# Performance work log

Measured on AMD Instinct MI355X. Metric: run time of the kernel, lower is better.

The kernel has to match this reference:

```python
import jax, jax.numpy as jnp
import numpy as np

# Module-level constants from the source
L = 6       # n_layer
NH = 6      # n_head
D = 96      # dim_emb
HS = D // NH  # head_size = 16
FF = 4 * D  # 384
DG, DO, DA = 32, 64, 16   # dim_goal, dim_obs, dim_act
T = 1024    # history_size (input_seq_size)
B = 16      # batch
STD = 0.02  # init std per _init_weights


def setup_inputs() -> dict:
    key = jax.random.key(0)
    ks = jax.random.split(key, 16)
    n = lambda k, s: jax.random.normal(k, s, dtype=jnp.float32) * STD
    return {
        "goals": jax.random.normal(ks[0], (B, 1, DG), dtype=jnp.float32),
        "obss": jax.random.normal(ks[1], (B, T, DO), dtype=jnp.float32),
        # goal_obs_embedding: Linear(DG+DO -> D), stored [in, out]
        "w_go": n(ks[2], (DG + DO, D)), "b_go": jnp.zeros((D,), jnp.float32),
        # input_position_embedding table [T, D]
        "pos_emb": n(ks[3], (T, D)),
        # per-layer, per-head Q/K/V projections (no bias): [L, NH, D, HS]
        "wq": n(ks[4], (L, NH, D, HS)),
        "wk": n(ks[5], (L, NH, D, HS)),
        "wv": n(ks[6], (L, NH, D, HS)),
        # output projection per layer: Linear(D -> D)
        "w_proj": n(ks[7], (L, D, D)), "b_proj": jnp.zeros((L, D), jnp.float32),
        # layernorms (init: weight=1, bias=0)
        "ln1_g": jnp.ones((L, D), jnp.float32), "ln1_b": jnp.zeros((L, D), jnp.float32),
        "ln2_g": jnp.ones((L, D), jnp.float32), "ln2_b": jnp.zeros((L, D), jnp.float32),
        # feedforward: Linear(D->4D), ReLU, Linear(4D->D)
        "w_ff1": n(ks[8], (L, D, FF)), "b_ff1": jnp.zeros((L, FF), jnp.float32),
        "w_ff2": n(ks[9], (L, FF, D)), "b_ff2": jnp.zeros((L, D), jnp.float32),
        # final layernorm + act_mean head
        "lnf_g": jnp.ones((D,), jnp.float32), "lnf_b": jnp.zeros((D,), jnp.float32),
        "w_act": n(ks[10], (D, DA)), "b_act": jnp.zeros((DA,), jnp.float32),
    }


def _layernorm(x, g, b):
    m = jnp.mean(x, axis=-1, keepdims=True)
    v = jnp.var(x, axis=-1, keepdims=True)
    return (x - m) * jax.lax.rsqrt(v + 1e-5) * g + b


def reference(goals, obss, w_go, b_go, pos_emb, wq, wk, wv, w_proj, b_proj,
              ln1_g, ln1_b, ln2_g, ln2_b, w_ff1, b_ff1, w_ff2, b_ff2,
              lnf_g, lnf_b, w_act, b_act):
    b, t, _ = obss.shape
    # goal_obs = cat([goals.repeat(1, H_in, 1), obss], -1) -> embed + pos
    goal_obs = jnp.concatenate([jnp.broadcast_to(goals, (b, t, DG)), obss], axis=-1)
    x = goal_obs @ w_go + b_go + pos_emb[:t]  # [B, T, D]
    mask = jnp.tril(jnp.ones((t, t), dtype=bool))  # causal tril buffer
    scale = HS ** -0.5
    for l in range(L):
        # --- multi-head causal self-attention (dropout = eval identity) ---
        xn = _layernorm(x, ln1_g[l], ln1_b[l])
        q = jnp.einsum('btd,hdk->bhtk', xn, wq[l])
        k = jnp.einsum('btd,hdk->bhtk', xn, wk[l])
        v = jnp.einsum('btd,hdk->bhtk', xn, wv[l])
        att = jnp.einsum('bhtk,bhsk->bhts', q, k) * scale  # [B, NH, T, T]
        att = jnp.where(mask, att, -jnp.inf)
        att = jax.nn.softmax(att, axis=-1)
        o = jnp.einsum('bhts,bhsk->bhtk', att, v)          # [B, NH, T, HS]
        o = o.transpose(0, 2, 1, 3).reshape(b, t, NH * HS)  # concat heads
        x = x + o @ w_proj[l] + b_proj[l]
        # --- feedforward ---
        xn = _layernorm(x, ln2_g[l], ln2_b[l])
        x = x + jax.nn.relu(xn @ w_ff1[l] + b_ff1[l]) @ w_ff2[l] + b_ff2[l]
    x = _layernorm(x, lnf_g, lnf_b)
    return x @ w_act + b_act  # act_mean, [B, T, DA]
```

## Files before the change

kernel.cpp:

```cpp
#include <hip/hip_runtime.h>
#include <math.h>

#define B_ 16
#define T_ 1024
#define D_ 96
#define L_ 6
#define NH_ 6
#define HS_ 16
#define FF_ 384

typedef _Float16 h4 __attribute__((ext_vector_type(4)));
typedef _Float16 h8 __attribute__((ext_vector_type(8)));
typedef __fp16 g2 __attribute__((ext_vector_type(2)));
typedef __fp16 g4 __attribute__((ext_vector_type(4)));
typedef float f4 __attribute__((ext_vector_type(4)));

#define MFMA16 __builtin_amdgcn_mfma_f32_16x16x16f16

#define OFF_GO   0
#define OFF_QKV  9216
#define OFF_PROJ 175104
#define OFF_FF1  230400
#define OFF_FF2  451584
#define OFF_ACT  672768
#define PACK_TOTAL 674304

#define QSCALE 0.3606737602222409f

static __device__ __forceinline__ h4 pk4(const float* p) {
  g2 lo = __builtin_amdgcn_cvt_pkrtz(p[0], p[1]);
  g2 hi = __builtin_amdgcn_cvt_pkrtz(p[2], p[3]);
  g4 r4 = __builtin_shufflevector(lo, hi, 0, 1, 2, 3);
  return __builtin_bit_cast(h4, r4);
}

static __device__ __forceinline__ void ldpair(const _Float16* base, int blk,
                                              int lane, h4& a, h4& b) {
  h8 t = *(const h8*)(base + (size_t)blk * 512 + lane * 8);
  a = __builtin_shufflevector(t, t, 0, 1, 2, 3);
  b = __builtin_shufflevector(t, t, 4, 5, 6, 7);
}

static __device__ __forceinline__ void ldkv(const _Float16* kB_, const _Float16* vB_,
                                            int tile, int lane,
                                            h4& k0, h4& k1, h4& v0, h4& v1) {
  h8 kt = *(const h8*)(kB_ + (size_t)tile * 512 + lane * 8);
  k0 = __builtin_shufflevector(kt, kt, 0, 1, 2, 3);
  k1 = __builtin_shufflevector(kt, kt, 4, 5, 6, 7);
  h8 vt = *(const h8*)(vB_ + (size_t)tile * 512 + lane * 8);
  v0 = __builtin_shufflevector(vt, vt, 0, 1, 2, 3);
  v1 = __builtin_shufflevector(vt, vt, 4, 5, 6, 7);
}

static __device__ __forceinline__ void astep_full(
    const h4& kc0, const h4& kc1, const h4& vc0, const h4& vc1,
    const h4& qf0, const h4& qf1, const h4& ones,
    f4& O0, f4& O1, f4& S0, f4& S1) {
  const f4 zero4 = {0.f, 0.f, 0.f, 0.f};
  f4 sa0 = MFMA16(kc0, qf0, zero4, 0, 0, 0);
  f4 sa1 = MFMA16(kc1, qf0, zero4, 0, 0, 0);
  f4 sb0 = MFMA16(kc0, qf1, zero4, 0, 0, 0);
  f4 sb1 = MFMA16(kc1, qf1, zero4, 0, 0, 0);
  float pa0[4], pa1[4], pb0[4], pb1[4];
#pragma unroll
  for (int r = 0; r < 4; ++r) {
    pa0[r] = __builtin_amdgcn_exp2f(sa0[r]);
    pa1[r] = __builtin_amdgcn_exp2f(sa1[r]);
    pb0[r] = __builtin_amdgcn_exp2f(sb0[r]);
    pb1[r] = __builtin_amdgcn_exp2f(sb1[r]);
  }
  h4 fa0 = pk4(pa0), fa1 = pk4(pa1), fb0 = pk4(pb0), fb1 = pk4(pb1);
  O0 = MFMA16(fa0, vc0, O0, 0, 0, 0);
  O0 = MFMA16(fa1, vc1, O0, 0, 0, 0);
  S0 = MFMA16(fa0, ones, S0, 0, 0, 0);
  S0 = MFMA16(fa1, ones, S0, 0, 0, 0);
  O1 = MFMA16(fb0, vc0, O1, 0, 0, 0);
  O1 = MFMA16(fb1, vc1, O1, 0, 0, 0);
  S1 = MFMA16(fb0, ones, S1, 0, 0, 0);
  S1 = MFMA16(fb1, ones, S1, 0, 0, 0);
}

static __device__ __forceinline__ void astep_diag(
    const h4& kc0, const h4& kc1, const h4& vc0, const h4& vc1,
    const h4& qf0, const h4& qf1, const h4& ones,
    f4& O0, f4& O1, f4& S0, f4& S1, int lr, int lg) {
  const f4 zero4 = {0.f, 0.f, 0.f, 0.f};
  f4 sa0 = MFMA16(kc0, qf0, zero4, 0, 0, 0);
  float pa0[4];
#pragma unroll
  for (int r = 0; r < 4; ++r)
    pa0[r] = (lg * 4 + r <= lr) ? __builtin_amdgcn_exp2f(sa0[r]) : 0.f;
  h4 fa0 = pk4(pa0);
  O0 = MFMA16(fa0, vc0, O0, 0, 0, 0);
  S0 = MFMA16(fa0, ones, S0, 0, 0, 0);
  f4 sb0 = MFMA16(kc0, qf1, zero4, 0, 0, 0);
  f4 sb1 = MFMA16(kc1, qf1, zero4, 0, 0, 0);
  float pb0[4], pb1[4];
#pragma unroll
  for (int r = 0; r < 4; ++r) {
    pb0[r] = __builtin_amdgcn_exp2f(sb0[r]);
    pb1[r] = (lg * 4 + r <= lr) ? __builtin_amdgcn_exp2f(sb1[r]) : 0.f;
  }
  h4 fb0 = pk4(pb0), fb1 = pk4(pb1);
  O1 = MFMA16(fb0, vc0, O1, 0, 0, 0);
  O1 = MFMA16(fb1, vc1, O1, 0, 0, 0);
  S1 = MFMA16(fb0, ones, S1, 0, 0, 0);
  S1 = MFMA16(fb1, ones, S1, 0, 0, 0);
}

__global__ __launch_bounds__(256) void pack_all_kernel(
    const float* __restrict__ w_go, const float* __restrict__ wq,
    const float* __restrict__ wk, const float* __restrict__ wv,
    const float* __restrict__ w_proj, const float* __restrict__ w_ff1,
    const float* __restrict__ w_ff2, const float* __restrict__ w_act,
    _Float16* __restrict__ P) {
  int i = blockIdx.x * 256 + threadIdx.x;
  if (i >= PACK_TOTAL) return;
  float v;
  if (i < OFF_QKV) {
    int o = i, nf = o / 1536, r = o % 1536, stp = r / 512, q = r & 511;
    int lane = q >> 3, h8i = q & 7, lr = lane & 15, lg = lane >> 4;
    int st = stp * 2 + (h8i >> 2), j = h8i & 3;
    int n = nf * 16 + lr, k = st * 16 + lg * 4 + j;
    v = w_go[k * 96 + n];
  } else if (i < OFF_PROJ) {
    int o = i - OFF_QKV, l = o / 27648, r0 = o % 27648;
    int nf = r0 / 1536, r = r0 % 1536, stp = r / 512, q = r & 511;
    int lane = q >> 3, h8i = q & 7, lr = lane & 15, lg = lane >> 4;
    int st = stp * 2 + (h8i >> 2), j = h8i & 3;
    int c = nf * 16 + lr, k = st * 16 + lg * 4 + j;
    int which = c / 96, hc = c % 96, h = hc >> 4, jx = hc & 15;
    const float* s = (which == 0) ? wq : (which == 1 ? wk : wv);
    v = s[((l * NH_ + h) * 96 + k) * 16 + jx];
    if (which == 0) v *= QSCALE;
  } else if (i < OFF_FF1) {
    int o = i - OFF_PROJ, l = o / 9216, r0 = o % 9216;
    int nf = r0 / 1536, r = r0 % 1536, stp = r / 512, q = r & 511;
    int lane = q >> 3, h8i = q & 7, lr = lane & 15, lg = lane >> 4;
    int st = stp * 2 + (h8i >> 2), j = h8i & 3;
    int n = nf * 16 + lr, k = st * 16 + lg * 4 + j;
    v = w_proj[l * 9216 + k * 96 + n];
  } else if (i < OFF_FF2) {
    int o = i - OFF_FF1, l = o / 36864, r0 = o % 36864;
    int nf = r0 / 1536, r = r0 % 1536, stp = r / 512, q = r & 511;
    int lane = q >> 3, h8i = q & 7, lr = lane & 15, lg = lane >> 4;
    int st = stp * 2 + (h8i >> 2), j = h8i & 3;
    int n = nf * 16 + lr, k = st * 16 + lg * 4 + j;
    v = w_ff1[l * 36864 + k * 384 + n];
  } else if (i < OFF_ACT) {
    int o = i - OFF_FF2, l = o / 36864, r0 = o % 36864;
    int nf = r0 / 6144, r = r0 % 6144, stp = r / 512, q = r & 511;
    int lane = q >> 3, h8i = q & 7, lr = lane & 15, lg = lane >> 4;
    int st = stp * 2 + (h8i >> 2), j = h8i & 3;
    int n = nf * 16 + lr, k = st * 16 + lg * 4 + j;
    v = w_ff2[l * 36864 + k * 96 + n];
  } else {
    int o = i - OFF_ACT, stp = o / 512, q = o & 511;
    int lane = q >> 3, h8i = q & 7, lr = lane & 15, lg = lane >> 4;
    int st = stp * 2 + (h8i >> 2), j = h8i & 3;
    int k = st * 16 + lg * 4 + j;
    v = w_act[k * 16 + lr];
  }
  P[i] = (_Float16)v;
}


__global__ __launch_bounds__(384, 1) void embed_kernel(
    const float* __restrict__ goals, const float* __restrict__ obss,
    const float* __restrict__ pos, const float* __restrict__ b_go,
    const _Float16* __restrict__ Wp, float* __restrict__ x,
    const float* __restrict__ lntg, const float* __restrict__ lntb,
    const _Float16* __restrict__ Wtail,
    _Float16* __restrict__ qp_, _Float16* __restrict__ kp_,
    _Float16* __restrict__ vp_) {
  __shared__ float smemf[16128];
#define XSH(g, row, c) ((_Float16*)smemf + (size_t)(g) * 1920 + (row) * 20 + (c))
#define LNS(g, w, r, i) smemf[15360 + (((g) * 6 + (w)) * 16 + (r)) * 2 + (i)]
#define XP(g) (x + ((size_t)(blockIdx.x * 4 + (g)) * 6 + cfo) * 256 + lane * 4)
  const int tid = threadIdx.x;
  const int wave = tid >> 6, lane = tid & 63;
  const int lr = lane & 15, lg = lane >> 4;
  const int b = blockIdx.x >> 4, jj = blockIdx.x & 15;
  const int cfo = wave;
  const f4 zero4 = {0.f, 0.f, 0.f, 0.f};
  int mrow[4] = {2 * jj, 2 * jj + 1, 62 - 2 * jj, 63 - 2 * jj};
  int tt_[4], t2_[4];
#pragma unroll
  for (int g = 0; g < 4; ++g) { tt_[g] = mrow[g] * 16 + lr; t2_[g] = (g < 2) ? jj : 31 - jj; }

  f4 xc[4];
  h4 ef[4][6];
#pragma unroll
  for (int st = 0; st < 2; ++st) {
    f4 s4 = *(const f4*)(goals + b * 32 + st * 16 + lg * 4);
    h4 e = (h4){(_Float16)s4[0], (_Float16)s4[1], (_Float16)s4[2], (_Float16)s4[3]};
#pragma unroll
    for (int g = 0; g < 4; ++g) ef[g][st] = e;
  }
#pragma unroll
  for (int g = 0; g < 4; ++g)
#pragma unroll
    for (int st = 2; st < 6; ++st) {
      f4 s4 = *(const f4*)(obss + (size_t)(b * 1024 + tt_[g]) * 64 +
                           (st - 2) * 16 + lg * 4);
      ef[g][st] = (h4){(_Float16)s4[0], (_Float16)s4[1], (_Float16)s4[2], (_Float16)s4[3]};
    }
  h4 wf[6];
#pragma unroll
  for (int stp = 0; stp < 3; ++stp)
    ldpair(Wp, cfo * 3 + stp, lane, wf[2 * stp], wf[2 * stp + 1]);
  f4 bb = *(const f4*)(b_go + cfo * 16 + lg * 4);
#pragma unroll
  for (int g = 0; g < 4; ++g) {
    f4 a = zero4;
#pragma unroll
    for (int st = 0; st < 6; ++st) a = MFMA16(wf[st], ef[g][st], a, 0, 0, 0);
    f4 pp = *(const f4*)(pos + (size_t)tt_[g] * 96 + cfo * 16 + lg * 4);
#pragma unroll
    for (int j = 0; j < 4; ++j) xc[g][j] = a[j] + bb[j] + pp[j];
    *(f4*)XP(g) = xc[g];
  }

#pragma unroll
  for (int g = 0; g < 4; ++g) {
    float s = xc[g][0] + xc[g][1] + xc[g][2] + xc[g][3];
    float sq = xc[g][0] * xc[g][0] + xc[g][1] * xc[g][1] +
               xc[g][2] * xc[g][2] + xc[g][3] * xc[g][3];
    s += __shfl_xor(s, 16); sq += __shfl_xor(sq, 16);
    s += __shfl_xor(s, 32); sq += __shfl_xor(sq, 32);
    if (lane < 16) { LNS(g, wave, lr, 0) = s; LNS(g, wave, lr, 1) = sq; }
  }
  __syncthreads();
  {
    f4 gg4 = *(const f4*)(lntg + cfo * 16 + lg * 4);
    f4 b4 = *(const f4*)(lntb + cfo * 16 + lg * 4);
#pragma unroll
    for (int g = 0; g < 4; ++g) {
      float s = 0.f, sq = 0.f;
#pragma unroll
      for (int w = 0; w < 6; ++w) { s += LNS(g, w, lr, 0); sq += LNS(g, w, lr, 1); }
      float mean = s * (1.f / 96.f);
      float rs = rsqrtf(sq * (1.f / 96.f) - mean * mean + 1e-5f);
      h4 xn;
#pragma unroll
      for (int j = 0; j < 4; ++j)
        xn[j] = (_Float16)((xc[g][j] - mean) * rs * gg4[j] + b4[j]);
      *(h4*)XSH(g, cfo * 16 + lr, lg * 4) = xn;
    }
  }
  __syncthreads();
  h4 xf[4][6];
#pragma unroll
  for (int g = 0; g < 4; ++g)
#pragma unroll
    for (int st = 0; st < 6; ++st)
      xf[g][st] = *(const h4*)XSH(g, st * 16 + lr, lg * 4);
#pragma unroll
  for (int f = 0; f < 3; ++f) {
    int nf = wave * 3 + f;
    h4 wt[6];
#pragma unroll
    for (int stp = 0; stp < 3; ++stp)
      ldpair(Wtail, nf * 3 + stp, lane, wt[2 * stp], wt[2 * stp + 1]);
#pragma unroll
    for (int g = 0; g < 4; ++g) {
      f4 a = zero4;
#pragma unroll
      for (int st = 0; st < 6; ++st) a = MFMA16(wt[st], xf[g][st], a, 0, 0, 0);
      if (nf < 12) {
        int h = nf < 6 ? nf : nf - 6;
        _Float16* dst = (nf < 6 ? qp_ : kp_) +
                        ((size_t)(b * NH_ + h) * 32 + t2_[g]) * 512 +
                        lane * 8 + (g & 1) * 4;
        h4 hv = {(_Float16)a[0], (_Float16)a[1], (_Float16)a[2], (_Float16)a[3]};
        *(h4*)dst = hv;
      } else {
        int hb = nf - 12;
        _Float16* vbase = vp_ + ((size_t)(b * NH_ + hb) * 32 + t2_[g]) * 512;
        int jb = (lr & 3) + (g & 1) * 4;
        int lgp = lr >> 2;
#pragma unroll
        for (int r = 0; r < 4; ++r)
          vbase[(lgp * 16 + lg * 4 + r) * 8 + jb] = (_Float16)a[r];
      }
    }
  }
#undef XSH
#undef LNS
#undef XP
}

template <bool HEAD>
__global__ __launch_bounds__(384, 1) void layer_kernel(
    const _Float16* __restrict__ Qs, const _Float16* __restrict__ Ks,
    const _Float16* __restrict__ Vs,
    const _Float16* __restrict__ Wp, const float* __restrict__ bp,
    float* __restrict__ x,
    const _Float16* __restrict__ W1, const float* __restrict__ b1,
    const _Float16* __restrict__ W2, const float* __restrict__ b2,
    const float* __restrict__ ln2g, const float* __restrict__ ln2b,
    const float* __restrict__ lntg, const float* __restrict__ lntb,
    const _Float16* __restrict__ Wtail, const float* __restrict__ btail,
    _Float16* __restrict__ qp_, _Float16* __restrict__ kp_,
    _Float16* __restrict__ vp_, float* __restrict__ out) {
  __shared__ float smemf[16128];
#define XSH(g, row, c) ((_Float16*)smemf + (size_t)(g) * 1920 + (row) * 20 + (c))
#define OSH ((_Float16*)smemf + 7680)
#define HSP(g, fp) ((_Float16*)smemf + ((size_t)(g) * 12 + (fp)) * 512)
#define LNS(g, w, r, i) smemf[15360 + (((g) * 6 + (w)) * 16 + (r)) * 2 + (i)]
#define XP(g) (x + ((size_t)(blockIdx.x * 4 + (g)) * 6 + cfo) * 256 + lane * 4)
  const int tid = threadIdx.x;
  const int wave = tid >> 6, lane = tid & 63;
  const int lr = lane & 15, lg = lane >> 4;
  const int b = blockIdx.x >> 4, jj = blockIdx.x & 15;
  const int cfo = wave;
  const f4 zero4 = {0.f, 0.f, 0.f, 0.f};
  const h4 ones = {(_Float16)1.f, (_Float16)1.f, (_Float16)1.f, (_Float16)1.f};
  int mrow[4] = {2 * jj, 2 * jj + 1, 62 - 2 * jj, 63 - 2 * jj};
  int tt_[4], tok_[4], t2_[4];
#pragma unroll
  for (int g = 0; g < 4; ++g) {
    tt_[g] = mrow[g] * 16 + lr;
    tok_[g] = b * 1024 + tt_[g];
    t2_[g] = (g < 2) ? jj : 31 - jj;
  }

  {
    const size_t bhoff = (size_t)(b * NH_ + wave) * 16384;
    const _Float16* qB_ = Qs + bhoff;
    const _Float16* kB_ = Ks + bhoff;
    const _Float16* vB_ = Vs + bhoff;
    const int qA = jj, qB2 = 31 - jj;
    h4 qfA0, qfA1, qfB0, qfB1;
    {
      h8 t = *(const h8*)(qB_ + (size_t)qA * 512 + lane * 8);
      qfA0 = __builtin_shufflevector(t, t, 0, 1, 2, 3);
      qfA1 = __builtin_shufflevector(t, t, 4, 5, 6, 7);
      h8 t2v = *(const h8*)(qB_ + (size_t)qB2 * 512 + lane * 8);
      qfB0 = __builtin_shufflevector(t2v, t2v, 0, 1, 2, 3);
      qfB1 = __builtin_shufflevector(t2v, t2v, 4, 5, 6, 7);
    }
    f4 OA0 = zero4, OA1 = zero4, SA0 = zero4, SA1 = zero4;
    f4 OB0 = zero4, OB1 = zero4, SB0 = zero4, SB1 = zero4;
    h4 kc0, kc1, vc0, vc1, kn0, kn1, vn0, vn1;
    ldkv(kB_, vB_, 0, lane, kc0, kc1, vc0, vc1);
    for (int t3 = 0; t3 < qA; ++t3) {
      ldkv(kB_, vB_, t3 + 1, lane, kn0, kn1, vn0, vn1);
      astep_full(kc0, kc1, vc0, vc1, qfA0, qfA1, ones, OA0, OA1, SA0, SA1);
      astep_full(kc0, kc1, vc0, vc1, qfB0, qfB1, ones, OB0, OB1, SB0, SB1);
      kc0 = kn0; kc1 = kn1; vc0 = vn0; vc1 = vn1;
    }
    {
      ldkv(kB_, vB_, qA + 1, lane, kn0, kn1, vn0, vn1);
      astep_diag(kc0, kc1, vc0, vc1, qfA0, qfA1, ones, OA0, OA1, SA0, SA1, lr, lg);
      astep_full(kc0, kc1, vc0, vc1, qfB0, qfB1, ones, OB0, OB1, SB0, SB1);
      kc0 = kn0; kc1 = kn1; vc0 = vn0; vc1 = vn1;
    }
    for (int t3 = qA + 1; t3 < qB2; ++t3) {
      ldkv(kB_, vB_, t3 + 1, lane, kn0, kn1, vn0, vn1);
      astep_full(kc0, kc1, vc0, vc1, qfB0, qfB1, ones, OB0, OB1, SB0, SB1);
      kc0 = kn0; kc1 = kn1; vc0 = vn0; vc1 = vn1;
    }
    astep_diag(kc0, kc1, vc0, vc1, qfB0, qfB1, ones, OB0, OB1, SB0, SB1, lr, lg);
    int stp = wave >> 1;
    int jb = (lr & 3) + (wave & 1) * 4;
    int lgp = lr >> 2;
#pragma unroll
    for (int r = 0; r < 4; ++r) {
      int pos = (lgp * 16 + lg * 4 + r) * 8 + jb;
      OSH[(0 * 3 + stp) * 512 + pos] = (_Float16)(OA0[r] * __builtin_amdgcn_rcpf(SA0[r]));
      OSH[(1 * 3 + stp) * 512 + pos] = (_Float16)(OA1[r] * __builtin_amdgcn_rcpf(SA1[r]));
      OSH[(2 * 3 + stp) * 512 + pos] = (_Float16)(OB0[r] * __builtin_amdgcn_rcpf(SB0[r]));
      OSH[(3 * 3 + stp) * 512 + pos] = (_Float16)(OB1[r] * __builtin_amdgcn_rcpf(SB1[r]));
    }
  }
  __syncthreads();

  f4 xc[4], x1[4];
  h4 obf[4][6];
#pragma unroll
  for (int g = 0; g < 4; ++g)
#pragma unroll
    for (int stp = 0; stp < 3; ++stp) {
      h8 t = *(const h8*)(OSH + ((size_t)(g * 3 + stp)) * 512 + lane * 8);
      obf[g][2 * stp] = __builtin_shufflevector(t, t, 0, 1, 2, 3);
      obf[g][2 * stp + 1] = __builtin_shufflevector(t, t, 4, 5, 6, 7);
    }
  h4 wf[6];
#pragma unroll
  for (int stp = 0; stp < 3; ++stp)
    ldpair(Wp, cfo * 3 + stp, lane, wf[2 * stp], wf[2 * stp + 1]);
  f4 bb = *(const f4*)(bp + cfo * 16 + lg * 4);
#pragma unroll
  for (int g = 0; g < 4; ++g) {
    f4 a = zero4;
#pragma unroll
    for (int st = 0; st < 6; ++st) a = MFMA16(wf[st], obf[g][st], a, 0, 0, 0);
    f4 xr = *(const f4*)XP(g);
#pragma unroll
    for (int j = 0; j < 4; ++j) x1[g][j] = a[j] + bb[j] + xr[j];
  }
#pragma unroll
  for (int g = 0; g < 4; ++g) {
    float s = x1[g][0] + x1[g][1] + x1[g][2] + x1[g][3];
    float sq = x1[g][0] * x1[g][0] + x1[g][1] * x1[g][1] +
               x1[g][2] * x1[g][2] + x1[g][3] * x1[g][3];
    s += __shfl_xor(s, 16); sq += __shfl_xor(sq, 16);
    s += __shfl_xor(s, 32); sq += __shfl_xor(sq, 32);
    if (lane < 16) { LNS(g, wave, lr, 0) = s; LNS(g, wave, lr, 1) = sq; }
  }
  __syncthreads();
  {
    f4 gg4 = *(const f4*)(ln2g + cfo * 16 + lg * 4);
    f4 b4 = *(const f4*)(ln2b + cfo * 16 + lg * 4);
#pragma unroll
    for (int g = 0; g < 4; ++g) {
      float s = 0.f, sq = 0.f;
#pragma unroll
      for (int w = 0; w < 6; ++w) { s += LNS(g, w, lr, 0); sq += LNS(g, w, lr, 1); }
      float mean = s * (1.f / 96.f);
      float rs = rsqrtf(sq * (1.f / 96.f) - mean * mean + 1e-5f);
      h4 xn;
#pragma unroll
      for (int j = 0; j < 4; ++j)
        xn[j] = (_Float16)((x1[g][j] - mean) * rs * gg4[j] + b4[j]);
      *(h4*)XSH(g, cfo * 16 + lr, lg * 4) = xn;
    }
  }
  __syncthreads();
  h4 xnf[4][6];
#pragma unroll
  for (int g = 0; g < 4; ++g)
#pragma unroll
    for (int st = 0; st < 6; ++st)
      xnf[g][st] = *(const h4*)XSH(g, st * 16 + lr, lg * 4);
  __syncthreads();

#pragma unroll
  for (int p = 0; p < 2; ++p) {
    int nf0 = wave * 4 + p * 2;
    h4 wA[6], wB[6];
#pragma unroll
    for (int stp = 0; stp < 3; ++stp) {
      ldpair(W1, nf0 * 3 + stp, lane, wA[2 * stp], wA[2 * stp + 1]);
      ldpair(W1, (nf0 + 1) * 3 + stp, lane, wB[2 * stp], wB[2 * stp + 1]);
    }
    f4 bA = *(const f4*)(b1 + nf0 * 16 + lg * 4);
    f4 bB = *(const f4*)(b1 + (nf0 + 1) * 16 + lg * 4);
#pragma unroll
    for (int g = 0; g < 4; ++g) {
      f4 hA = zero4, hB = zero4;
#pragma unroll
      for (int st = 0; st < 6; ++st) {
        hA = MFMA16(wA[st], xnf[g][st], hA, 0, 0, 0);
        hB = MFMA16(wB[st], xnf[g][st], hB, 0, 0, 0);
      }
      h4 lo, hi;
#pragma unroll
      for (int j = 0; j < 4; ++j) {
        lo[j] = (_Float16)fmaxf(hA[j] + bA[j], 0.f);
        hi[j] = (_Float16)fmaxf(hB[j] + bB[j], 0.f);
      }
      h8 comb = __builtin_shufflevector(lo, hi, 0, 1, 2, 3, 4, 5, 6, 7);
      *(h8*)(HSP(g, wave * 2 + p) + lane * 8) = comb;
    }
  }
  h4 w2f[24];
#pragma unroll
  for (int stp = 0; stp < 12; ++stp)
    ldpair(W2, cfo * 12 + stp, lane, w2f[2 * stp], w2f[2 * stp + 1]);
  __syncthreads();
  {
    f4 b4 = *(const f4*)(b2 + cfo * 16 + lg * 4);
#pragma unroll
    for (int g = 0; g < 4; ++g) {
      f4 y = zero4;
#pragma unroll
      for (int fp = 0; fp < 12; ++fp) {
        h8 t = *(const h8*)(HSP(g, fp) + lane * 8);
        h4 lo = __builtin_shufflevector(t, t, 0, 1, 2, 3);
        h4 hi = __builtin_shufflevector(t, t, 4, 5, 6, 7);
        y = MFMA16(w2f[2 * fp], lo, y, 0, 0, 0);
        y = MFMA16(w2f[2 * fp + 1], hi, y, 0, 0, 0);
      }
#pragma unroll
      for (int j = 0; j < 4; ++j) xc[g][j] = x1[g][j] + y[j] + b4[j];
      if constexpr (!HEAD)
        *(f4*)XP(g) = xc[g];
    }
  }

#pragma unroll
  for (int g = 0; g < 4; ++g) {
    float s = xc[g][0] + xc[g][1] + xc[g][2] + xc[g][3];
    float sq = xc[g][0] * xc[g][0] + xc[g][1] * xc[g][1] +
               xc[g][2] * xc[g][2] + xc[g][3] * xc[g][3];
    s += __shfl_xor(s, 16); sq += __shfl_xor(sq, 16);
    s += __shfl_xor(s, 32); sq += __shfl_xor(sq, 32);
    if (lane < 16) { LNS(g, wave, lr, 0) = s; LNS(g, wave, lr, 1) = sq; }
  }
  __syncthreads();
  {
    f4 gg4 = *(const f4*)(lntg + cfo * 16 + lg * 4);
    f4 b4 = *(const f4*)(lntb + cfo * 16 + lg * 4);
#pragma unroll
    for (int g = 0; g < 4; ++g) {
      float s = 0.f, sq = 0.f;
#pragma unroll
      for (int w = 0; w < 6; ++w) { s += LNS(g, w, lr, 0); sq += LNS(g, w, lr, 1); }
      float mean = s * (1.f / 96.f);
      float rs = rsqrtf(sq * (1.f / 96.f) - mean * mean + 1e-5f);
      h4 xn;
#pragma unroll
      for (int j = 0; j < 4; ++j)
        xn[j] = (_Float16)((xc[g][j] - mean) * rs * gg4[j] + b4[j]);
      *(h4*)XSH(g, cfo * 16 + lr, lg * 4) = xn;
    }
  }
  __syncthreads();
  if constexpr (HEAD) {
    if (wave == 0) {
      h4 wt[6];
#pragma unroll
      for (int stp = 0; stp < 3; ++stp)
        ldpair(Wtail, stp, lane, wt[2 * stp], wt[2 * stp + 1]);
      f4 bbt = *(const f4*)(btail + lg * 4);
#pragma unroll
      for (int g = 0; g < 4; ++g) {
        f4 a = zero4;
#pragma unroll
        for (int st = 0; st < 6; ++st) {
          h4 xf = *(const h4*)XSH(g, st * 16 + lr, lg * 4);
          a = MFMA16(wt[st], xf, a, 0, 0, 0);
        }
        f4 o;
#pragma unroll
        for (int j = 0; j < 4; ++j) o[j] = a[j] + bbt[j];
        *(f4*)(out + (size_t)tok_[g] * 16 + lg * 4) = o;
      }
    }
  } else {
    h4 xf[4][6];
#pragma unroll
    for (int g = 0; g < 4; ++g)
#pragma unroll
      for (int st = 0; st < 6; ++st)
        xf[g][st] = *(const h4*)XSH(g, st * 16 + lr, lg * 4);
#pragma unroll
    for (int f = 0; f < 3; ++f) {
      int nf = wave * 3 + f;
      h4 wt[6];
#pragma unroll
      for (int stp = 0; stp < 3; ++stp)
        ldpair(Wtail, nf * 3 + stp, lane, wt[2 * stp], wt[2 * stp + 1]);
#pragma unroll
      for (int g = 0; g < 4; ++g) {
        f4 a = zero4;
#pragma unroll
        for (int st = 0; st < 6; ++st) a = MFMA16(wt[st], xf[g][st], a, 0, 0, 0);
        if (nf < 12) {
          int h = nf < 6 ? nf : nf - 6;
          _Float16* dst = (nf < 6 ? qp_ : kp_) +
                          ((size_t)(b * NH_ + h) * 32 + t2_[g]) * 512 +
                          lane * 8 + (g & 1) * 4;
          h4 hv = {(_Float16)a[0], (_Float16)a[1], (_Float16)a[2], (_Float16)a[3]};
          *(h4*)dst = hv;
        } else {
          int hb = nf - 12;
          _Float16* vbase = vp_ + ((size_t)(b * NH_ + hb) * 32 + t2_[g]) * 512;
          int jb = (lr & 3) + (g & 1) * 4;
          int lgp = lr >> 2;
#pragma unroll
          for (int r = 0; r < 4; ++r)
            vbase[(lgp * 16 + lg * 4 + r) * 8 + jb] = (_Float16)a[r];
        }
      }
    }
  }
#undef XSH
#undef OSH
#undef HSP
#undef LNS
#undef XP
}

extern "C" void kernel_launch(void* const* d_in, const int* in_sizes, int n_in,
                              void* d_out, int out_size, void* d_ws, size_t ws_size,
                              hipStream_t stream) {
  const float* goals   = (const float*)d_in[0];
  const float* obss    = (const float*)d_in[1];
  const float* w_go    = (const float*)d_in[2];
  const float* b_go    = (const float*)d_in[3];
  const float* pos_emb = (const float*)d_in[4];
  const float* wq      = (const float*)d_in[5];
  const float* wk      = (const float*)d_in[6];
  const float* wv      = (const float*)d_in[7];
  const float* w_proj  = (const float*)d_in[8];
  const float* b_proj  = (const float*)d_in[9];
  const float* ln1_g   = (const float*)d_in[10];
  const float* ln1_b   = (const float*)d_in[11];
  const float* ln2_g   = (const float*)d_in[12];
  const float* ln2_b   = (const float*)d_in[13];
  const float* w_ff1   = (const float*)d_in[14];
  const float* b_ff1   = (const float*)d_in[15];
  const float* w_ff2   = (const float*)d_in[16];
  const float* b_ff2   = (const float*)d_in[17];
  const float* lnf_g   = (const float*)d_in[18];
  const float* lnf_b   = (const float*)d_in[19];
  const float* w_act   = (const float*)d_in[20];
  const float* b_act   = (const float*)d_in[21];
  float* out = (float*)d_out;

  const int M = B_ * T_;
  float* ws = (float*)d_ws;
  size_t off = 0;
  _Float16* P = (_Float16*)(ws + off); off += PACK_TOTAL / 2 + 64;
  float* x = ws + off; off += (size_t)M * 96;
  _Float16* Qb[2]; _Float16* Kb[2]; _Float16* Vb[2];
  for (int p = 0; p < 2; ++p) {
    Qb[p] = (_Float16*)(ws + off); off += (size_t)M * 48;
    Kb[p] = (_Float16*)(ws + off); off += (size_t)M * 48;
    Vb[p] = (_Float16*)(ws + off); off += (size_t)M * 48;
  }

  pack_all_kernel<<<(PACK_TOTAL + 255) / 256, 256, 0, stream>>>(
      w_go, wq, wk, wv, w_proj, w_ff1, w_ff2, w_act, P);

  embed_kernel<<<256, 384, 0, stream>>>(
      goals, obss, pos_emb, b_go, P + OFF_GO, x, ln1_g, ln1_b,
      P + OFF_QKV, Qb[0], Kb[0], Vb[0]);

  for (int l = 0; l < L_; ++l) {
    int sp = l & 1, dp = (l + 1) & 1;
    if (l < L_ - 1) {
      layer_kernel<false><<<256, 384, 0, stream>>>(
          Qb[sp], Kb[sp], Vb[sp],
          P + OFF_PROJ + (size_t)l * 9216, b_proj + l * 96, x,
          P + OFF_FF1 + (size_t)l * 36864, b_ff1 + l * 384,
          P + OFF_FF2 + (size_t)l * 36864, b_ff2 + l * 96,
          ln2_g + l * 96, ln2_b + l * 96,
          ln1_g + (l + 1) * 96, ln1_b + (l + 1) * 96,
          P + OFF_QKV + (size_t)(l + 1) * 27648, nullptr,
          Qb[dp], Kb[dp], Vb[dp], nullptr);
    } else {
      layer_kernel<true><<<256, 384, 0, stream>>>(
          Qb[sp], Kb[sp], Vb[sp],
          P + OFF_PROJ + (size_t)l * 9216, b_proj + l * 96, x,
          P + OFF_FF1 + (size_t)l * 36864, b_ff1 + l * 384,
          P + OFF_FF2 + (size_t)l * 36864, b_ff2 + l * 96,
          ln2_g + l * 96, ln2_b + l * 96,
          lnf_g, lnf_b, P + OFF_ACT, b_act,
          nullptr, nullptr, nullptr, out);
    }
  }
}
```

Baseline: 186.3 us.

## Fuse six per-layer launches into one cooperative persistent kernel with grid sync

Replaces the six per-layer kernel launches with a single cooperative kernel that loops over the layers. Between layers it issues a threadfence and a grid-wide sync, with Q/K/V buffers ping-ponged through pointer selection. The goal is to remove per-launch overhead and the gaps between kernels. The cost is a grid barrier per layer, and it relies on all 256 blocks being co-resident; the launch return value is not checked.

```diff
diff --git a/kernel.cpp b/kernel.cpp
--- a/kernel.cpp
+++ b/kernel.cpp
@@ -1,5 +1,8 @@
 #include <hip/hip_runtime.h>
+#include <hip/hip_cooperative_groups.h>
 #include <math.h>
+
+namespace cg = cooperative_groups;
 
 #define B_ 16
 #define T_ 1024
@@ -164,7 +167,6 @@
   P[i] = (_Float16)v;
 }
 
-
 __global__ __launch_bounds__(384, 1) void embed_kernel(
     const float* __restrict__ goals, const float* __restrict__ obss,
     const float* __restrict__ pos, const float* __restrict__ b_go,
@@ -290,25 +292,25 @@
 #undef XP
 }
 
-template <bool HEAD>
-__global__ __launch_bounds__(384, 1) void layer_kernel(
-    const _Float16* __restrict__ Qs, const _Float16* __restrict__ Ks,
-    const _Float16* __restrict__ Vs,
-    const _Float16* __restrict__ Wp, const float* __restrict__ bp,
-    float* __restrict__ x,
-    const _Float16* __restrict__ W1, const float* __restrict__ b1,
-    const _Float16* __restrict__ W2, const float* __restrict__ b2,
-    const float* __restrict__ ln2g, const float* __restrict__ ln2b,
-    const float* __restrict__ lntg, const float* __restrict__ lntb,
-    const _Float16* __restrict__ Wtail, const float* __restrict__ btail,
-    _Float16* __restrict__ qp_, _Float16* __restrict__ kp_,
-    _Float16* __restrict__ vp_, float* __restrict__ out) {
+__global__ __launch_bounds__(384, 1) void all_layers_kernel(
+    const _Float16* __restrict__ P,
+    const float* __restrict__ b_proj,
+    const float* __restrict__ ln1_g, const float* __restrict__ ln1_b,
+    const float* __restrict__ ln2_g, const float* __restrict__ ln2_b,
+    const float* __restrict__ b_ff1, const float* __restrict__ b_ff2,
+    const float* __restrict__ lnf_g, const float* __restrict__ lnf_b,
+    const float* __restrict__ b_act, float* __restrict__ x,
+    _Float16* __restrict__ Q0, _Float16* __restrict__ K0,
+    _Float16* __restrict__ V0, _Float16* __restrict__ Q1,
+    _Float16* __restrict__ K1, _Float16* __restrict__ V1,
+    float* __restrict__ out) {
   __shared__ float smemf[16128];
 #define XSH(g, row, c) ((_Float16*)smemf + (size_t)(g) * 1920 + (row) * 20 + (c))
 #define OSH ((_Float16*)smemf + 7680)
 #define HSP(g, fp) ((_Float16*)smemf + ((size_t)(g) * 12 + (fp)) * 512)
 #define LNS(g, w, r, i) smemf[15360 + (((g) * 6 + (w)) * 16 + (r)) * 2 + (i)]
 #define XP(g) (x + ((size_t)(blockIdx.x * 4 + (g)) * 6 + cfo) * 256 + lane * 4)
+  cg::grid_group grid = cg::this_grid();
   const int tid = threadIdx.x;
   const int wave = tid >> 6, lane = tid & 63;
   const int lr = lane & 15, lg = lane >> 4;
@@ -325,256 +327,282 @@
     t2_[g] = (g < 2) ? jj : 31 - jj;
   }
 
-  {
-    const size_t bhoff = (size_t)(b * NH_ + wave) * 16384;
-    const _Float16* qB_ = Qs + bhoff;
-    const _Float16* kB_ = Ks + bhoff;
-    const _Float16* vB_ = Vs + bhoff;
-    const int qA = jj, qB2 = 31 - jj;
-    h4 qfA0, qfA1, qfB0, qfB1;
+  for (int l = 0; l < L_; ++l) {
+    const bool last = (l == L_ - 1);
+    const _Float16* Qs = (l & 1) ? Q1 : Q0;
+    const _Float16* Ks = (l & 1) ? K1 : K0;
+    const _Float16* Vs = (l & 1) ? V1 : V0;
+    _Float16* qp_ = (l & 1) ? Q0 : Q1;
+    _Float16* kp_ = (l & 1) ? K0 : K1;
+    _Float16* vp_ = (l & 1) ? V0 : V1;
+    const _Float16* Wp = P + OFF_PROJ + (size_t)l * 9216;
+    const float* bp = b_proj + l * 96;
+    const _Float16* W1 = P + OFF_FF1 + (size_t)l * 36864;
+    const float* b1 = b_ff1 + l * 384;
+    const _Float16* W2 = P + OFF_FF2 + (size_t)l * 36864;
+    const float* b2 = b_ff2 + l * 96;
+    const float* ln2g = ln2_g + l * 96;
+    const float* ln2b = ln2_b + l * 96;
+    const float* lntg = last ? lnf_g : ln1_g + (l + 1) * 96;
+    const float* lntb = last ? lnf_b : ln1_b + (l + 1) * 96;
+    const _Float16* Wtail = last ? (P + OFF_ACT)
+                                 : (P + OFF_QKV + (size_t)(l + 1) * 27648);
+
     {
-      h8 t = *(const h8*)(qB_ + (size_t)qA * 512 + lane * 8);
-      qfA0 = __builtin_shufflevector(t, t, 0, 1, 2, 3);
-      qfA1 = __builtin_shufflevector(t, t, 4, 5, 6, 7);
-      h8 t2v = *(const h8*)(qB_ + (size_t)qB2 * 512 + lane * 8);
-      qfB0 = __builtin_shufflevector(t2v, t2v, 0, 1, 2, 3);
-      qfB1 = __builtin_shufflevector(t2v, t2v, 4, 5, 6, 7);
-    }
-    f4 OA0 = zero4, OA1 = zero4, SA0 = zero4, SA1 = zero4;
-    f4 OB0 = zero4, OB1 = zero4, SB0 = zero4, SB1 = zero4;
-    h4 kc0, kc1, vc0, vc1, kn0, kn1, vn0, vn1;
-    ldkv(kB_, vB_, 0, lane, kc0, kc1, vc0, vc1);
-    for (int t3 = 0; t3 < qA; ++t3) {
-      ldkv(kB_, vB_, t3 + 1, lane, kn0, kn1, vn0, vn1);
-      astep_full(kc0, kc1, vc0, vc1, qfA0, qfA1, ones, OA0, OA1, SA0, SA1);
-      astep_full(kc0, kc1, vc0, vc1, qfB0, qfB1, ones, OB0, OB1, SB0, SB1);
-      kc0 = kn0; kc1 = kn1; vc0 = vn0; vc1 = vn1;
-    }
+      const size_t bhoff = (size_t)(b * NH_ + wave) * 16384;
+      const _Float16* qB_ = Qs + bhoff;
+      const _Float16* kB_ = Ks + bhoff;
+      const _Float16* vB_ = Vs + bhoff;
+      const int qA = jj, qB2 = 31 - jj;
+      h4 qfA0, qfA1, qfB0, qfB1;
+      {
+        h8 t = *(const h8*)(qB_ + (size_t)qA * 512 + lane * 8);
+        qfA0 = __builtin_shufflevector(t, t, 0, 1, 2, 3);
+        qfA1 = __builtin_shufflevector(t, t, 4, 5, 6, 7);
+        h8 t2v = *(const h8*)(qB_ + (size_t)qB2 * 512 + lane * 8);
+        qfB0 = __builtin_shufflevector(t2v, t2v, 0, 1, 2, 3);
+        qfB1 = __builtin_shufflevector(t2v, t2v, 4, 5, 6, 7);
+      }
+      f4 OA0 = zero4, OA1 = zero4, SA0 = zero4, SA1 = zero4;
+      f4 OB0 = zero4, OB1 = zero4, SB0 = zero4, SB1 = zero4;
+      h4 kc0, kc1, vc0, vc1, kn0, kn1, vn0, vn1;
+      ldkv(kB_, vB_, 0, lane, kc0, kc1, vc0, vc1);
+      for (int t3 = 0; t3 < qA; ++t3) {
+        ldkv(kB_, vB_, t3 + 1, lane, kn0, kn1, vn0, vn1);
+        astep_full(kc0, kc1, vc0, vc1, qfA0, qfA1, ones, OA0, OA1, SA0, SA1);
+        astep_full(kc0, kc1, vc0, vc1, qfB0, qfB1, ones, OB0, OB1, SB0, SB1);
+        kc0 = kn0; kc1 = kn1; vc0 = vn0; vc1 = vn1;
+      }
+      {
+        ldkv(kB_, vB_, qA + 1, lane, kn0, kn1, vn0, vn1);
+        astep_diag(kc0, kc1, vc0, vc1, qfA0, qfA1, ones, OA0, OA1, SA0, SA1, lr, lg);
+        astep_full(kc0, kc1, vc0, vc1, qfB0, qfB1, ones, OB0, OB1, SB0, SB1);
+        kc0 = kn0; kc1 = kn1; vc0 = vn0; vc1 = vn1;
+      }
+      for (int t3 = qA + 1; t3 < qB2; ++t3) {
+        ldkv(kB_, vB_, t3 + 1, lane, kn0, kn1, vn0, vn1);
+        astep_full(kc0, kc1, vc0, vc1, qfB0, qfB1, ones, OB0, OB1, SB0, SB1);
+        kc0 = kn0; kc1 = kn1; vc0 = vn0; vc1 = vn1;
+      }
+      astep_diag(kc0, kc1, vc0, vc1, qfB0, qfB1, ones, OB0, OB1, SB0, SB1, lr, lg);
+      int stp = wave >> 1;
+      int jb = (lr & 3) + (wave & 1) * 4;
+      int lgp = lr >> 2;
+#pragma unroll
+      for (int r = 0; r < 4; ++r) {
+        int pos = (lgp * 16 + lg * 4 + r) * 8 + jb;
+        OSH[(0 * 3 + stp) * 512 + pos] = (_Float16)(OA0[r] * __builtin_amdgcn_rcpf(SA0[r]));
+        OSH[(1 * 3 + stp) * 512 + pos] = (_Float16)(OA1[r] * __builtin_amdgcn_rcpf(SA1[r]));
+        OSH[(2 * 3 + stp) * 512 + pos] = (_Float16)(OB0[r] * __builtin_amdgcn_rcpf(SB0[r]));
+        OSH[(3 * 3 + stp) * 512 + pos] = (_Float16)(OB1[r] * __builtin_amdgcn_rcpf(SB1[r]));
+      }
+    }
+    __syncthreads();
+
+    f4 xc[4], x1[4];
+    h4 obf[4][6];
+#pragma unroll
+    for (int g = 0; g < 4; ++g)
+#pragma unroll
+      for (int stp = 0; stp < 3; ++stp) {
+        h8 t = *(const h8*)(OSH + ((size_t)(g * 3 + stp)) * 512 + lane * 8);
+        obf[g][2 * stp] = __builtin_shufflevector(t, t, 0, 1, 2, 3);
+        obf[g][2 * stp + 1] = __builtin_shufflevector(t, t, 4, 5, 6, 7);
+      }
+    h4 wf[6];
+#pragma unroll
+    for (int stp = 0; stp < 3; ++stp)
+      ldpair(Wp, cfo * 3 + stp, lane, wf[2 * stp], wf[2 * stp + 1]);
+    f4 bb = *(const f4*)(bp + cfo * 16 + lg * 4);
+#pragma unroll
+    for (int g = 0; g < 4; ++g) {
+      f4 a = zero4;
+#pragma unroll
+      for (int st = 0; st < 6; ++st) a = MFMA16(wf[st], obf[g][st], a, 0, 0, 0);
+      f4 xr = *(const f4*)XP(g);
+#pragma unroll
+      for (int j = 0; j < 4; ++j) x1[g][j] = a[j] + bb[j] + xr[j];
+    }
+#pragma unroll
+    for (int g = 0; g < 4; ++g) {
+      float s = x1[g][0] + x1[g][1] + x1[g][2] + x1[g][3];
+      float sq = x1[g][0] * x1[g][0] + x1[g][1] * x1[g][1] +
+                 x1[g][2] * x1[g][2] + x1[g][3] * x1[g][3];
+      s += __shfl_xor(s, 16); sq += __shfl_xor(sq, 16);
+      s += __shfl_xor(s, 32); sq += __shfl_xor(sq, 32);
+      if (lane < 16) { LNS(g, wave, lr, 0) = s; LNS(g, wave, lr, 1) = sq; }
+    }
+    __syncthreads();
     {
-      ldkv(kB_, vB_, qA + 1, lane, kn0, kn1, vn0, vn1);
-      astep_diag(kc0, kc1, vc0, vc1, qfA0, qfA1, ones, OA0, OA1, SA0, SA1, lr, lg);
-      astep_full(kc0, kc1, vc0, vc1, qfB0, qfB1, ones, OB0, OB1, SB0, SB1);
-      kc0 = kn0; kc1 = kn1; vc0 = vn0; vc1 = vn1;
-    }
-    for (int t3 = qA + 1; t3 < qB2; ++t3) {
-      ldkv(kB_, vB_, t3 + 1, lane, kn0, kn1, vn0, vn1);
-      astep_full(kc0, kc1, vc0, vc1, qfB0, qfB1, ones, OB0, OB1, SB0, SB1);
-      kc0 = kn0; kc1 = kn1; vc0 = vn0; vc1 = vn1;
-    }
-    astep_diag(kc0, kc1, vc0, vc1, qfB0, qfB1, ones, OB0, OB1, SB0, SB1, lr, lg);
-    int stp = wave >> 1;
-    int jb = (lr & 3) + (wave & 1) * 4;
-    int lgp = lr >> 2;
-#pragma unroll
-    for (int r = 0; r < 4; ++r) {
-      int pos = (lgp * 16 + lg * 4 + r) * 8 + jb;
-      OSH[(0 * 3 + stp) * 512 + pos] = (_Float16)(OA0[r] * __builtin_amdgcn_rcpf(SA0[r]));
-      OSH[(1 * 3 + stp) * 512 + pos] = (_Float16)(OA1[r] * __builtin_amdgcn_rcpf(SA1[r]));
-      OSH[(2 * 3 + stp) * 512 + pos] = (_Float16)(OB0[r] * __builtin_amdgcn_rcpf(SB0[r]));
-      OSH[(3 * 3 + stp) * 512 + pos] = (_Float16)(OB1[r] * __builtin_amdgcn_rcpf(SB1[r]));
-    }
-  }
-  __syncthreads();
-
-  f4 xc[4], x1[4];
-  h4 obf[4][6];
-#pragma unroll
-  for (int g = 0; g < 4; ++g)
-#pragma unroll
-    for (int stp = 0; stp < 3; ++stp) {
-      h8 t = *(const h8*)(OSH + ((size_t)(g * 3 + stp)) * 512 + lane * 8);
-      obf[g][2 * stp] = __builtin_shufflevector(t, t, 0, 1, 2, 3);
-      obf[g][2 * stp + 1] = __builtin_shufflevector(t, t, 4, 5, 6, 7);
-    }
-  h4 wf[6];
-#pragma unroll
-  for (int stp = 0; stp < 3; ++stp)
-    ldpair(Wp, cfo * 3 + stp, lane, wf[2 * stp], wf[2 * stp + 1]);
-  f4 bb = *(const f4*)(bp + cfo * 16 + lg * 4);
-#pragma unroll
-  for (int g = 0; g < 4; ++g) {
-    f4 a = zero4;
-#pragma unroll
-    for (int st = 0; st < 6; ++st) a = MFMA16(wf[st], obf[g][st], a, 0, 0, 0);
-    f4 xr = *(const f4*)XP(g);
-#pragma unroll
-    for (int j = 0; j < 4; ++j) x1[g][j] = a[j] + bb[j] + xr[j];
-  }
-#pragma unroll
-  for (int g = 0; g < 4; ++g) {
-    float s = x1[g][0] + x1[g][1] + x1[g][2] + x1[g][3];
-    float sq = x1[g][0] * x1[g][0] + x1[g][1] * x1[g][1] +
-               x1[g][2] * x1[g][2] + x1[g][3] * x1[g][3];
-    s += __shfl_xor(s, 16); sq += __shfl_xor(sq, 16);
-    s += __shfl_xor(s, 32); sq += __shfl_xor(sq, 32);
-    if (lane < 16) { LNS(g, wave, lr, 0) = s; LNS(g, wave, lr, 1) = sq; }
-  }
-  __syncthreads();
-  {
-    f4 gg4 = *(const f4*)(ln2g + cfo * 16 + lg * 4);
-    f4 b4 = *(const f4*)(ln2b + cfo * 16 + lg * 4);
+      f4 gg4 = *(const f4*)(ln2g + cfo * 16 + lg * 4);
+      f4 b4 = *(const f4*)(ln2b + cfo * 16 + lg * 4);
+#pragma unroll
+      for (int g = 0; g < 4; ++g) {
+        float s = 0.f, sq = 0.f;
+#pragma unroll
+        for (int w = 0; w < 6; ++w) { s += LNS(g, w, lr, 0); sq += LNS(g, w, lr, 1); }
+        float mean = s * (1.f / 96.f);
+        float rs = rsqrtf(sq * (1.f / 96.f) - mean * mean + 1e-5f);
+        h4 xn;
+#pragma unroll
+        for (int j = 0; j < 4; ++j)
+          xn[j] = (_Float16)((x1[g][j] - mean) * rs * gg4[j] + b4[j]);
+        *(h4*)XSH(g, cfo * 16 + lr, lg * 4) = xn;
+      }
+    }
+    __syncthreads();
+    h4 xnf[4][6];
+#pragma unroll
+    for (int g = 0; g < 4; ++g)
+#pragma unroll
+      for (int st = 0; st < 6; ++st)
+        xnf[g][st] = *(const h4*)XSH(g, st * 16 + lr, lg * 4);
+    __syncthreads();
+
+#pragma unroll
+    for (int p = 0; p < 2; ++p) {
+      int nf0 = wave * 4 + p * 2;
+      h4 wA[6], wB[6];
+#pragma unroll
+      for (int stp = 0; stp < 3; ++stp) {
+        ldpair(W1, nf0 * 3 + stp, lane, wA[2 * stp], wA[2 * stp + 1]);
+        ldpair(W1, (nf0 + 1) * 3 + stp, lane, wB[2 * stp], wB[2 * stp + 1]);
+      }
+      f4 bA = *(const f4*)(b1 + nf0 * 16 + lg * 4);
+      f4 bB = *(const f4*)(b1 + (nf0 + 1) * 16 + lg * 4);
+#pragma unroll
+      for (int g = 0; g < 4; ++g) {
+        f4 hA = zero4, hB = zero4;
+#pragma unroll
+        for (int st = 0; st < 6; ++st) {
+          hA = MFMA16(wA[st], xnf[g][st], hA, 0, 0, 0);
+          hB = MFMA16(wB[st], xnf[g][st], hB, 0, 0, 0);
+        }
+        h4 lo, hi;
+#pragma unroll
+        for (int j = 0; j < 4; ++j) {
+          lo[j] = (_Float16)fmaxf(hA[j] + bA[j], 0.f);
+          hi[j] = (_Float16)fmaxf(hB[j] + bB[j], 0.f);
+        }
+        h8 comb = __builtin_shufflevector(lo, hi, 0, 1, 2, 3, 4, 5, 6, 7);
+        *(h8*)(HSP(g, wave * 2 + p) + lane * 8) = comb;
+      }
+    }
+    h4 w2f[24];
+#pragma unroll
+    for (int stp = 0; stp < 12; ++stp)
+      ldpair(W2, cfo * 12 + stp, lane, w2f[2 * stp], w2f[2 * stp + 1]);
+    __syncthreads();
+    {
+      f4 b4 = *(const f4*)(b2 + cfo * 16 + lg * 4);
+#pragma unroll
+      for (int g = 0; g < 4; ++g) {
+        f4 y = zero4;
+#pragma unroll
+        for (int fp = 0; fp < 12; ++fp) {
+          h8 t = *(const h8*)(HSP(g, fp) + lane * 8);
+          h4 lo = __builtin_shufflevector(t, t, 0, 1, 2, 3);
+          h4 hi = __builtin_shufflevector(t, t, 4, 5, 6, 7);
+          y = MFMA16(w2f[2 * fp], lo, y, 0, 0, 0);
+          y = MFMA16(w2f[2 * fp + 1], hi, y, 0, 0, 0);
+        }
+#pragma unroll
+        for (int j = 0; j < 4; ++j) xc[g][j] = x1[g][j] + y[j] + b4[j];
+        if (!last) *(f4*)XP(g) = xc[g];
+      }
+    }
+
 #pragma unroll
     for (int g = 0; g < 4; ++g) {
-      float s = 0.f, sq = 0.f;
-#pragma unroll
-      for (int w = 0; w < 6; ++w) { s += LNS(g, w, lr, 0); sq += LNS(g, w, lr, 1); }
-      float mean = s * (1.f / 96.f);
-      float rs = rsqrtf(sq * (1.f / 96.f) - mean * mean + 1e-5f);
-      h4 xn;
-#pragma unroll
-      for (int j = 0; j < 4; ++j)
-        xn[j] = (_Float16)((x1[g][j] - mean) * rs * gg4[j] + b4[j]);
-      *(h4*)XSH(g, cfo * 16 + lr, lg * 4) = xn;
-    }
-  }
-  __syncthreads();
-  h4 xnf[4][6];
-#pragma unroll
-  for (int g = 0; g < 4; ++g)
-#pragma unroll
-    for (int st = 0; st < 6; ++st)
-      xnf[g][st] = *(const h4*)XSH(g, st * 16 + lr, lg * 4);
-  __syncthreads();
-
-#pragma unroll
-  for (int p = 0; p < 2; ++p) {
-    int nf0 = wave * 4 + p * 2;
-    h4 wA[6], wB[6];
-#pragma unroll
-    for (int stp = 0; stp < 3; ++stp) {
-      ldpair(W1, nf0 * 3 + stp, lane, wA[2 * stp], wA[2 * stp + 1]);
-      ldpair(W1, (nf0 + 1) * 3 + stp, lane, wB[2 * stp], wB[2 * stp + 1]);
-    }
-    f4 bA = *(const f4*)(b1 + nf0 * 16 + lg * 4);
-    f4 bB = *(const f4*)(b1 + (nf0 + 1) * 16 + lg * 4);
-#pragma unroll
-    for (int g = 0; g < 4; ++g) {
-      f4 hA = zero4, hB = zero4;
-#pragma unroll
-      for (int st = 0; st < 6; ++st) {
-        hA = MFMA16(wA[st], xnf[g][st], hA, 0, 0, 0);
-        hB = MFMA16(wB[st], xnf[g][st], hB, 0, 0, 0);
-      }
-      h4 lo, hi;
-#pragma unroll
-      for (int j = 0; j < 4; ++j) {
-        lo[j] = (_Float16)fmaxf(hA[j] + bA[j], 0.f);
-        hi[j] = (_Float16)fmaxf(hB[j] + bB[j], 0.f);
-      }
-      h8 comb = __builtin_shufflevector(lo, hi, 0, 1, 2, 3, 4, 5, 6, 7);
-      *(h8*)(HSP(g, wave * 2 + p) + lane * 8) = comb;
-    }
-  }
-  h4 w2f[24];
-#pragma unroll
-  for (int stp = 0; stp < 12; ++stp)
-    ldpair(W2, cfo * 12 + stp, lane, w2f[2 * stp], w2f[2 * stp + 1]);
-  __syncthreads();
-  {
-    f4 b4 = *(const f4*)(b2 + cfo * 16 + lg * 4);
-#pragma unroll
-    for (int g = 0; g < 4; ++g) {
-      f4 y = zero4;
-#pragma unroll
-      for (int fp = 0; fp < 12; ++fp) {
-        h8 t = *(const h8*)(HSP(g, fp) + lane * 8);
-        h4 lo = __builtin_shufflevector(t, t, 0, 1, 2, 3);
-        h4 hi = __builtin_shufflevector(t, t, 4, 5, 6, 7);
-        y = MFMA16(w2f[2 * fp], lo, y, 0, 0, 0);
-        y = MFMA16(w2f[2 * fp + 1], hi, y, 0, 0, 0);
-      }
-#pragma unroll
-      for (int j = 0; j < 4; ++j) xc[g][j] = x1[g][j] + y[j] + b4[j];
-      if constexpr (!HEAD)
-        *(f4*)XP(g) = xc[g];
-    }
-  }
-
-#pragma unroll
-  for (int g = 0; g < 4; ++g) {
-    float s = xc[g][0] + xc[g][1] + xc[g][2] + xc[g][3];
-    float sq = xc[g][0] * xc[g][0] + xc[g][1] * xc[g][1] +
-               xc[g][2] * xc[g][2] + xc[g][3] * xc[g][3];
-    s += __shfl_xor(s, 16); sq += __shfl_xor(sq, 16);
-    s += __shfl_xor(s, 32); sq += __shfl_xor(sq, 32);
-    if (lane < 16) { LNS(g, wave, lr, 0) = s; LNS(g, wave, lr, 1) = sq; }
-  }
-  __syncthreads();
-  {
-    f4 gg4 = *(const f4*)(lntg + cfo * 16 + lg * 4);
-    f4 b4 = *(const f4*)(lntb + cfo * 16 + lg * 4);
-#pragma unroll
-    for (int g = 0; g < 4; ++g) {
-      float s = 0.f, sq = 0.f;
-#pragma unroll
-      for (int w = 0; w < 6; ++w) { s += LNS(g, w, lr, 0); sq += LNS(g, w, lr, 1); }
-      float mean = s * (1.f / 96.f);
-      float rs = rsqrtf(sq * (1.f / 96.f) - mean * mean + 1e-5f);
-      h4 xn;
-#pragma unroll
-      for (int j = 0; j < 4; ++j)
-        xn[j] = (_Float16)((xc[g][j] - mean) * rs * gg4[j] + b4[j]);
-      *(h4*)XSH(g, cfo * 16 + lr, lg * 4) = xn;
-    }
-  }
-  __syncthreads();
-  if constexpr (HEAD) {
-    if (wave == 0) {
-      h4 wt[6];
-#pragma unroll
-      for (int stp = 0; stp < 3; ++stp)
-        ldpair(Wtail, stp, lane, wt[2 * stp], wt[2 * stp + 1]);
-      f4 bbt = *(const f4*)(btail + lg * 4);
+      float s = xc[g][0] + xc[g][1] + xc[g][2] + xc[g][3];
+      float sq = xc[g][0] * xc[g][0] + xc[g][1] * xc[g][1] +
+                 xc[g][2] * xc[g][2] + xc[g][3] * xc[g][3];
+      s += __shfl_xor(s, 16); sq += __shfl_xor(sq, 16);
+      s += __shfl_xor(s, 32); sq += __shfl_xor(sq, 32);
+      if (lane < 16) { LNS(g, wave, lr, 0) = s; LNS(g, wave, lr, 1) = sq; }
+    }
+    __syncthreads();
+    {
+      f4 gg4 = *(const f4*)(lntg + cfo * 16 + lg * 4);
+      f4 b4 = *(const f4*)(lntb + cfo * 16 + lg * 4);
 #pragma unroll
       for (int g = 0; g < 4; ++g) {
-        f4 a = zero4;
-#pragma unroll
-        for (int st = 0; st < 6; ++st) {
-          h4 xf = *(const h4*)XSH(g, st * 16 + lr, lg * 4);
-          a = MFMA16(wt[st], xf, a, 0, 0, 0);
+        float s = 0.f, sq = 0.f;
+#pragma unroll
+        for (int w = 0; w < 6; ++w) { s += LNS(g, w, lr, 0); sq += LNS(g, w, lr, 1); }
+        float mean = s * (1.f / 96.f);
+        float rs = rsqrtf(sq * (1.f / 96.f) - mean * mean + 1e-5f);
+        h4 xn;
+#pragma unroll
+        for (int j = 0; j < 4; ++j)
+          xn[j] = (_Float16)((xc[g][j] - mean) * rs * gg4[j] + b4[j]);
+        *(h4*)XSH(g, cfo * 16 + lr, lg * 4) = xn;
+      }
+    }
+    __syncthreads();
+    if (last) {
+      if (wave == 0) {
+        h4 wt[6];
+#pragma unroll
+        for (int stp = 0; stp < 3; ++stp)
+          ldpair(Wtail, stp, lane, wt[2 * stp], wt[2 * stp + 1]);
+        f4 bbt = *(const f4*)(b_act + lg * 4);
+#pragma unroll
+        for (int g = 0; g < 4; ++g) {
+          f4 a = zero4;
+#pragma unroll
+          for (int st = 0; st < 6; ++st) {
+            h4 xf = *(const h4*)XSH(g, st * 16 + lr, lg * 4);
+            a = MFMA16(wt[st], xf, a, 0, 0, 0);
+          }
+          f4 o;
+#pragma unroll
+          for (int j = 0; j < 4; ++j) o[j] = a[j] + bbt[j];
+          *(f4*)(out + (size_t)tok_[g] * 16 + lg * 4) = o;
         }
-        f4 o;
-#pragma unroll
-        for (int j = 0; j < 4; ++j) o[j] = a[j] + bbt[j];
-        *(f4*)(out + (size_t)tok_[g] * 16 + lg * 4) = o;
-      }
-    }
-  } else {
-    h4 xf[4][6];
-#pragma unroll
-    for (int g = 0; g < 4; ++g)
-#pragma unroll
-      for (int st = 0; st < 6; ++st)
-        xf[g][st] = *(const h4*)XSH(g, st * 16 + lr, lg * 4);
-#pragma unroll
-    for (int f = 0; f < 3; ++f) {
-      int nf = wave * 3 + f;
-      h4 wt[6];
-#pragma unroll
-      for (int stp = 0; stp < 3; ++stp)
-        ldpair(Wtail, nf * 3 + stp, lane, wt[2 * stp], wt[2 * stp + 1]);
-#pragma unroll
-      for (int g = 0; g < 4; ++g) {
-        f4 a = zero4;
-#pragma unroll
-        for (int st = 0; st < 6; ++st) a = MFMA16(wt[st], xf[g][st], a, 0, 0, 0);
-        if (nf < 12) {
-          int h = nf < 6 ? nf : nf - 6;
-          _Float16* dst = (nf < 6 ? qp_ : kp_) +
-                          ((size_t)(b * NH_ + h) * 32 + t2_[g]) * 512 +
-                          lane * 8 + (g & 1) * 4;
-          h4 hv = {(_Float16)a[0], (_Float16)a[1], (_Float16)a[2], (_Float16)a[3]};
-          *(h4*)dst = hv;
-        } else {
-          int hb = nf - 12;
-          _Float16* vbase = vp_ + ((size_t)(b * NH_ + hb) * 32 + t2_[g]) * 512;
-          int jb = (lr & 3) + (g & 1) * 4;
-          int lgp = lr >> 2;
-#pragma unroll
-          for (int r = 0; r < 4; ++r)
-            vbase[(lgp * 16 + lg * 4 + r) * 8 + jb] = (_Float16)a[r];
+      }
+    } else {
+      h4 xf[4][6];
+#pragma unroll
+      for (int g = 0; g < 4; ++g)
+#pragma unroll
+        for (int st = 0; st < 6; ++st)
+          xf[g][st] = *(const h4*)XSH(g, st * 16 + lr, lg * 4);
+#pragma unroll
+      for (int f = 0; f < 3; ++f) {
+        int nf = wave * 3 + f;
+        h4 wt[6];
+#pragma unroll
+        for (int stp = 0; stp < 3; ++stp)
+          ldpair(Wtail, nf * 3 + stp, lane, wt[2 * stp], wt[2 * stp + 1]);
+#pragma unroll
+        for (int g = 0; g < 4; ++g) {
+          f4 a = zero4;
+#pragma unroll
+          for (int st = 0; st < 6; ++st) a = MFMA16(wt[st], xf[g][st], a, 0, 0, 0);
+          if (nf < 12) {
+            int h = nf < 6 ? nf : nf - 6;
+            _Float16* dst = (nf < 6 ? qp_ : kp_) +
+                            ((size_t)(b * NH_ + h) * 32 + t2_[g]) * 512 +
+                            lane * 8 + (g & 1) * 4;
+            h4 hv = {(_Float16)a[0], (_Float16)a[1], (_Float16)a[2], (_Float16)a[3]};
+            *(h4*)dst = hv;
+          } else {
+            int hb = nf - 12;
+            _Float16* vbase = vp_ + ((size_t)(b * NH_ + hb) * 32 + t2_[g]) * 512;
+            int jb = (lr & 3) + (g & 1) * 4;
+            int lgp = lr >> 2;
+#pragma unroll
+            for (int r = 0; r < 4; ++r)
+              vbase[(lgp * 16 + lg * 4 + r) * 8 + jb] = (_Float16)a[r];
+          }
         }
       }
+    }
+    if (!last) {
+      __threadfence();
+      grid.sync();
+      __syncthreads();
     }
   }
 #undef XSH
@@ -630,27 +658,15 @@
       goals, obss, pos_emb, b_go, P + OFF_GO, x, ln1_g, ln1_b,
       P + OFF_QKV, Qb[0], Kb[0], Vb[0]);
 
-  for (int l = 0; l < L_; ++l) {
-    int sp = l & 1, dp = (l + 1) & 1;
-    if (l < L_ - 1) {
-      layer_kernel<false><<<256, 384, 0, stream>>>(
-          Qb[sp], Kb[sp], Vb[sp],
-          P + OFF_PROJ + (size_t)l * 9216, b_proj + l * 96, x,
-          P + OFF_FF1 + (size_t)l * 36864, b_ff1 + l * 384,
-          P + OFF_FF2 + (size_t)l * 36864, b_ff2 + l * 96,
-          ln2_g + l * 96, ln2_b + l * 96,
-          ln1_g + (l + 1) * 96, ln1_b + (l + 1) * 96,
-          P + OFF_QKV + (size_t)(l + 1) * 27648, nullptr,
-          Qb[dp], Kb[dp], Vb[dp], nullptr);
-    } else {
-      layer_kernel<true><<<256, 384, 0, stream>>>(
-          Qb[sp], Kb[sp], Vb[sp],
-          P + OFF_PROJ + (size_t)l * 9216, b_proj + l * 96, x,
-          P + OFF_FF1 + (size_t)l * 36864, b_ff1 + l * 384,
-          P + OFF_FF2 + (size_t)l * 36864, b_ff2 + l * 96,
-          ln2_g + l * 96, ln2_b + l * 96,
-          lnf_g, lnf_b, P + OFF_ACT, b_act,
-          nullptr, nullptr, nullptr, out);
-    }
-  }
-}
+  {
+    void* args[] = {
+      (void*)&P, (void*)&b_proj, (void*)&ln1_g, (void*)&ln1_b,
+      (void*)&ln2_g, (void*)&ln2_b, (void*)&b_ff1, (void*)&b_ff2,
+      (void*)&lnf_g, (void*)&lnf_b, (void*)&b_act, (void*)&x,
+      (void*)&Qb[0], (void*)&Kb[0], (void*)&Vb[0],
+      (void*)&Qb[1], (void*)&Kb[1], (void*)&Vb[1], (void*)&out,
+    };
+    hipLaunchCooperativeKernel((const void*)all_layers_kernel, dim3(256),
+                               dim3(384), args, 0, stream);
+  }
+}
```

Measured after the change: 593.7 us. +218.7%, slower.
